# Kernel optimization log

Hardware: AMD Instinct MI355X
Metric: run time of the kernel (lower is better)

## Reference

```python
import jax, jax.numpy as jnp
import numpy as np

N_NODES = 50000
N_EDGES = 800000
H = 8            # n_heads
VAL_CH = 64      # h * n value channels
D = 3            # SO(3) degree dimension (2l+1, l=1)
T = 16           # key dim per head


def setup_inputs() -> dict:
    key = jax.random.key(0)
    k1, k2, k3, k4 = jax.random.split(key, 4)
    v = jax.random.normal(k1, (N_EDGES, VAL_CH, D), dtype=jnp.float32)
    k = jax.random.normal(k2, (N_EDGES, H, T), dtype=jnp.float32)
    q = jax.random.normal(k3, (N_NODES, H, T), dtype=jnp.float32)
    dst = jax.random.randint(k4, (N_EDGES,), 0, N_NODES, dtype=jnp.int32)
    return {"v": v, "k": k, "q": q, "dst": dst}


def reference(v, k, q, dst):
    # v: [E, h*n, d] edge values; k: [E, h, t] edge keys; q: [N, h, t] node queries
    E = v.shape[0]
    N = q.shape[0]
    h = k.shape[1]
    t = k.shape[2]
    vh = v.reshape(E, h, -1, v.shape[-1])          # [E, h, n, d]
    scale = 1.0 / np.sqrt(h * t).astype(np.float32)  # sqrt(f_key.deg_size)
    # per-edge attention logits: dot(k_e, q_dst(e)) per head
    logits = jnp.einsum('eht,eht->eh', k, q[dst]) * scale   # [E, h]
    # edge softmax over incoming edges of each destination node
    m = jax.ops.segment_max(logits, dst, num_segments=N)    # [N, h]
    m = jax.lax.stop_gradient(m)
    ex = jnp.exp(logits - m[dst])                           # [E, h]
    denom = jax.ops.segment_sum(ex, dst, num_segments=N)    # [N, h]
    a = ex / denom[dst]                                     # [E, h]
    # weighted message + scatter-sum to destination nodes
    msg = a[:, :, None, None] * vh                          # [E, h, n, d]
    out = jax.ops.segment_sum(msg, dst, num_segments=N)     # [N, h, n, d]
    return out.reshape(N, -1, v.shape[-1])                  # [N, h*n, d]
```

## Files before the change

kernel.cpp:

```cpp
#include <hip/hip_runtime.h>

#define HH 8
#define CAPL 128
#define BSTRIDE 256

static constexpr float SCALE = 0.08838834764831843f;

struct f3 {
  float x, y, z;
};

__device__ __forceinline__ float dot16(const float* kp, float4 q0, float4 q1,
                                       float4 q2, float4 q3) {
  const float4* k4 = (const float4*)kp;
  float4 a = k4[0], b = k4[1], c = k4[2], d = k4[3];
  float acc = a.x * q0.x + a.y * q0.y + a.z * q0.z + a.w * q0.w;
  acc += b.x * q1.x + b.y * q1.y + b.z * q1.z + b.w * q1.w;
  acc += c.x * q2.x + c.y * q2.y + c.z * q2.z + c.w * q2.w;
  acc += d.x * q3.x + d.y * q3.y + d.z * q3.z + d.w * q3.w;
  return acc;
}

__global__ __launch_bounds__(256) void fill_kernel(const int* __restrict__ dst,
                                                   int* __restrict__ cursor,
                                                   int* __restrict__ eid,
                                                   int E) {
  int e = blockIdx.x * blockDim.x + threadIdx.x;
  if (e >= E) return;
  int d = dst[e];
  int pos = atomicAdd(&cursor[d], 1);
  if (pos < BSTRIDE) eid[(size_t)d * BSTRIDE + pos] = e;
}

__global__ __launch_bounds__(256) void node_kernel(
    const float* __restrict__ v, const float* __restrict__ k,
    const float* __restrict__ q, const int* __restrict__ cursor,
    const int* __restrict__ eid, float* __restrict__ out, int N) {
  __shared__ int eidL[4][CAPL];
  __shared__ float wL[4][CAPL * HH];
  __shared__ float ovfL[4][HH];

  int tid = threadIdx.x;
  int wave = tid >> 6;
  int lane = tid & 63;
  int node = blockIdx.x * 4 + wave;
  if (node >= N) return;

  int deg = cursor[node];
  int nl = min(deg, CAPL);
  int nb = min(deg, BSTRIDE);
  const int* bucket = eid + (size_t)node * BSTRIDE;

  for (int i = lane; i < nl; i += 64) eidL[wave][i] = bucket[i];

  int h = lane & 7;
  int j = lane >> 3;

  const float4* qq = (const float4*)(q + (size_t)node * 128 + h * 16);
  float4 q0 = qq[0], q1 = qq[1], q2 = qq[2], q3 = qq[3];

  float m = -1e30f;
  for (int i = j; i < nl; i += 8) {
    int e = eidL[wave][i];
    float lg = dot16(k + (size_t)e * 128 + h * 16, q0, q1, q2, q3) * SCALE;
    wL[wave][i * 8 + h] = lg;
    m = fmaxf(m, lg);
  }
  for (int i = CAPL + j; i < nb; i += 8) {
    int e = bucket[i];
    float lg = dot16(k + (size_t)e * 128 + h * 16, q0, q1, q2, q3) * SCALE;
    m = fmaxf(m, lg);
  }
  m = fmaxf(m, __shfl_xor(m, 8, 64));
  m = fmaxf(m, __shfl_xor(m, 16, 64));
  m = fmaxf(m, __shfl_xor(m, 32, 64));

  float s = 0.f;
  for (int i = j; i < nl; i += 8) {
    float ex = __expf(wL[wave][i * 8 + h] - m);
    wL[wave][i * 8 + h] = ex;
    s += ex;
  }
  for (int i = CAPL + j; i < nb; i += 8) {
    int e = bucket[i];
    float lg = dot16(k + (size_t)e * 128 + h * 16, q0, q1, q2, q3) * SCALE;
    s += __expf(lg - m);
  }
  s += __shfl_xor(s, 8, 64);
  s += __shfl_xor(s, 16, 64);
  s += __shfl_xor(s, 32, 64);
  float inv = (s > 0.f) ? 1.0f / s : 0.f;

  int hc = lane >> 3;
  float minv = __shfl(inv, hc, 64);
  float a0 = 0.f, a1 = 0.f, a2 = 0.f;
  for (int i = 0; i < nl; ++i) {
    int e = eidL[wave][i];
    float w = wL[wave][i * 8 + hc];
    f3 vv = *(const f3*)(v + (size_t)e * 192 + lane * 3);
    a0 += w * vv.x;
    a1 += w * vv.y;
    a2 += w * vv.z;
  }
  for (int i = CAPL; i < nb; ++i) {
    int e = bucket[i];
    if (lane < 8) {
      float lg = dot16(k + (size_t)e * 128 + lane * 16, q0, q1, q2, q3) * SCALE;
      ovfL[wave][lane] = __expf(lg - m);
    }
    float w = ovfL[wave][hc];
    f3 vv = *(const f3*)(v + (size_t)e * 192 + lane * 3);
    a0 += w * vv.x;
    a1 += w * vv.y;
    a2 += w * vv.z;
  }
  a0 *= minv;
  a1 *= minv;
  a2 *= minv;

  f3* op = (f3*)(out + (size_t)node * 192 + lane * 3);
  op->x = a0;
  op->y = a1;
  op->z = a2;
}

extern "C" void kernel_launch(void* const* d_in, const int* in_sizes, int n_in,
                              void* d_out, int out_size, void* d_ws,
                              size_t ws_size, hipStream_t stream) {
  const float* v = (const float*)d_in[0];
  const float* k = (const float*)d_in[1];
  const float* q = (const float*)d_in[2];
  const int* dst = (const int*)d_in[3];
  float* out = (float*)d_out;

  const int E = in_sizes[3];
  const int N = in_sizes[2] / (HH * 16);

  char* ws = (char*)d_ws;
  int* cursor = (int*)ws;
  int* eid = (int*)(ws + (((size_t)N * 4 + 255) & ~(size_t)255));

  hipMemsetAsync(cursor, 0, (size_t)N * sizeof(int), stream);
  fill_kernel<<<(E + 255) / 256, 256, 0, stream>>>(dst, cursor, eid, E);
  node_kernel<<<(N + 3) / 4, 256, 0, stream>>>(v, k, q, cursor, eid, out, N);
}
```

Baseline: 310.5 us.

## Compute edge logits in bucket-fill kernel and store them per node slot

Per-edge attention logits are now computed in the bucketing kernel, with 8 threads per edge reading k contiguously via nontemporal loads, and written into a per-node slot array. The node kernel then reads those logits as coalesced data instead of gathering k rows by edge id and recomputing dot products, including for overflow edges. The value accumulation loop is also unrolled by four, using 32-bit offset arithmetic. The cost is an extra logit buffer written and read back (N*256*8 floats of workspace), and the overflow path is now simpler.

```diff
diff --git a/kernel.cpp b/kernel.cpp
--- a/kernel.cpp
+++ b/kernel.cpp
@@ -10,35 +10,48 @@
   float x, y, z;
 };
 
-__device__ __forceinline__ float dot16(const float* kp, float4 q0, float4 q1,
-                                       float4 q2, float4 q3) {
-  const float4* k4 = (const float4*)kp;
-  float4 a = k4[0], b = k4[1], c = k4[2], d = k4[3];
-  float acc = a.x * q0.x + a.y * q0.y + a.z * q0.z + a.w * q0.w;
-  acc += b.x * q1.x + b.y * q1.y + b.z * q1.z + b.w * q1.w;
-  acc += c.x * q2.x + c.y * q2.y + c.z * q2.z + c.w * q2.w;
-  acc += d.x * q3.x + d.y * q3.y + d.z * q3.z + d.w * q3.w;
-  return acc;
-}
+typedef float vf4 __attribute__((ext_vector_type(4)));
 
-__global__ __launch_bounds__(256) void fill_kernel(const int* __restrict__ dst,
-                                                   int* __restrict__ cursor,
-                                                   int* __restrict__ eid,
-                                                   int E) {
-  int e = blockIdx.x * blockDim.x + threadIdx.x;
+__global__ __launch_bounds__(256) void edge_kernel(
+    const float* __restrict__ k, const float* __restrict__ q,
+    const int* __restrict__ dst, int* __restrict__ cursor,
+    int* __restrict__ eid, float* __restrict__ lgS, int E) {
+  int t = blockIdx.x * 256 + threadIdx.x;
+  int e = t >> 3;
   if (e >= E) return;
+  int h = t & 7;
+  int lane = threadIdx.x & 63;
   int d = dst[e];
-  int pos = atomicAdd(&cursor[d], 1);
-  if (pos < BSTRIDE) eid[(size_t)d * BSTRIDE + pos] = e;
+
+  const vf4* kk = (const vf4*)(k + (size_t)e * 128 + h * 16);
+  const vf4* qq = (const vf4*)(q + (size_t)d * 128 + h * 16);
+  vf4 a0 = __builtin_nontemporal_load(kk + 0);
+  vf4 a1 = __builtin_nontemporal_load(kk + 1);
+  vf4 a2 = __builtin_nontemporal_load(kk + 2);
+  vf4 a3 = __builtin_nontemporal_load(kk + 3);
+  vf4 b0 = qq[0], b1 = qq[1], b2 = qq[2], b3 = qq[3];
+  float acc = a0.x * b0.x + a0.y * b0.y + a0.z * b0.z + a0.w * b0.w;
+  acc += a1.x * b1.x + a1.y * b1.y + a1.z * b1.z + a1.w * b1.w;
+  acc += a2.x * b2.x + a2.y * b2.y + a2.z * b2.z + a2.w * b2.w;
+  acc += a3.x * b3.x + a3.y * b3.y + a3.z * b3.z + a3.w * b3.w;
+  float lg = acc * SCALE;
+
+  int pos = 0;
+  if (h == 0) pos = atomicAdd(&cursor[d], 1);
+  pos = __shfl(pos, lane & ~7, 64);
+  if (pos < BSTRIDE) {
+    size_t slot = (size_t)d * BSTRIDE + pos;
+    if (h == 0) eid[slot] = e;
+    lgS[slot * HH + h] = lg;
+  }
 }
 
 __global__ __launch_bounds__(256) void node_kernel(
-    const float* __restrict__ v, const float* __restrict__ k,
-    const float* __restrict__ q, const int* __restrict__ cursor,
-    const int* __restrict__ eid, float* __restrict__ out, int N) {
+    const float* __restrict__ v, const float* __restrict__ lgS,
+    const int* __restrict__ cursor, const int* __restrict__ eid,
+    float* __restrict__ out, int N) {
   __shared__ int eidL[4][CAPL];
   __shared__ float wL[4][CAPL * HH];
-  __shared__ float ovfL[4][HH];
 
   int tid = threadIdx.x;
   int wave = tid >> 6;
@@ -46,46 +59,35 @@
   int node = blockIdx.x * 4 + wave;
   if (node >= N) return;
 
-  int deg = cursor[node];
+  int deg = min(cursor[node], BSTRIDE);
   int nl = min(deg, CAPL);
-  int nb = min(deg, BSTRIDE);
   const int* bucket = eid + (size_t)node * BSTRIDE;
+  const float* lgN = lgS + (size_t)node * (BSTRIDE * HH);
+  const char* vB = (const char*)v;
+  uint32_t vlane = (uint32_t)(lane * 12);
 
   for (int i = lane; i < nl; i += 64) eidL[wave][i] = bucket[i];
 
-  int h = lane & 7;
-  int j = lane >> 3;
-
-  const float4* qq = (const float4*)(q + (size_t)node * 128 + h * 16);
-  float4 q0 = qq[0], q1 = qq[1], q2 = qq[2], q3 = qq[3];
-
   float m = -1e30f;
-  for (int i = j; i < nl; i += 8) {
-    int e = eidL[wave][i];
-    float lg = dot16(k + (size_t)e * 128 + h * 16, q0, q1, q2, q3) * SCALE;
-    wL[wave][i * 8 + h] = lg;
+  for (int i = lane; i < nl * 8; i += 64) {
+    float lg = lgN[i];
+    wL[wave][i] = lg;
     m = fmaxf(m, lg);
   }
-  for (int i = CAPL + j; i < nb; i += 8) {
-    int e = bucket[i];
-    float lg = dot16(k + (size_t)e * 128 + h * 16, q0, q1, q2, q3) * SCALE;
-    m = fmaxf(m, lg);
-  }
+  for (int i = CAPL * 8 + lane; i < deg * 8; i += 64)
+    m = fmaxf(m, lgN[i]);
   m = fmaxf(m, __shfl_xor(m, 8, 64));
   m = fmaxf(m, __shfl_xor(m, 16, 64));
   m = fmaxf(m, __shfl_xor(m, 32, 64));
 
   float s = 0.f;
-  for (int i = j; i < nl; i += 8) {
-    float ex = __expf(wL[wave][i * 8 + h] - m);
-    wL[wave][i * 8 + h] = ex;
+  for (int i = lane; i < nl * 8; i += 64) {
+    float ex = __expf(wL[wave][i] - m);
+    wL[wave][i] = ex;
     s += ex;
   }
-  for (int i = CAPL + j; i < nb; i += 8) {
-    int e = bucket[i];
-    float lg = dot16(k + (size_t)e * 128 + h * 16, q0, q1, q2, q3) * SCALE;
-    s += __expf(lg - m);
-  }
+  for (int i = CAPL * 8 + lane; i < deg * 8; i += 64)
+    s += __expf(lgN[i] - m);
   s += __shfl_xor(s, 8, 64);
   s += __shfl_xor(s, 16, 64);
   s += __shfl_xor(s, 32, 64);
@@ -93,23 +95,38 @@
 
   int hc = lane >> 3;
   float minv = __shfl(inv, hc, 64);
+  float m_c = __shfl(m, hc, 64);
   float a0 = 0.f, a1 = 0.f, a2 = 0.f;
-  for (int i = 0; i < nl; ++i) {
+  int i = 0;
+  for (; i + 4 <= nl; i += 4) {
+    int e0 = eidL[wave][i + 0];
+    int e1 = eidL[wave][i + 1];
+    int e2 = eidL[wave][i + 2];
+    int e3 = eidL[wave][i + 3];
+    float w0 = wL[wave][(i + 0) * 8 + hc];
+    float w1 = wL[wave][(i + 1) * 8 + hc];
+    float w2 = wL[wave][(i + 2) * 8 + hc];
+    float w3 = wL[wave][(i + 3) * 8 + hc];
+    f3 v0 = *(const f3*)(vB + (uint32_t)e0 * 768u + vlane);
+    f3 v1 = *(const f3*)(vB + (uint32_t)e1 * 768u + vlane);
+    f3 v2 = *(const f3*)(vB + (uint32_t)e2 * 768u + vlane);
+    f3 v3 = *(const f3*)(vB + (uint32_t)e3 * 768u + vlane);
+    a0 += w0 * v0.x + w1 * v1.x + w2 * v2.x + w3 * v3.x;
+    a1 += w0 * v0.y + w1 * v1.y + w2 * v2.y + w3 * v3.y;
+    a2 += w0 * v0.z + w1 * v1.z + w2 * v2.z + w3 * v3.z;
+  }
+  for (; i < nl; ++i) {
     int e = eidL[wave][i];
     float w = wL[wave][i * 8 + hc];
-    f3 vv = *(const f3*)(v + (size_t)e * 192 + lane * 3);
+    f3 vv = *(const f3*)(vB + (uint32_t)e * 768u + vlane);
     a0 += w * vv.x;
     a1 += w * vv.y;
     a2 += w * vv.z;
   }
-  for (int i = CAPL; i < nb; ++i) {
+  for (; i < deg; ++i) {
     int e = bucket[i];
-    if (lane < 8) {
-      float lg = dot16(k + (size_t)e * 128 + lane * 16, q0, q1, q2, q3) * SCALE;
-      ovfL[wave][lane] = __expf(lg - m);
-    }
-    float w = ovfL[wave][hc];
-    f3 vv = *(const f3*)(v + (size_t)e * 192 + lane * 3);
+    float w = __expf(lgN[i * 8 + hc] - m_c);
+    f3 vv = *(const f3*)(vB + (uint32_t)e * 768u + vlane);
     a0 += w * vv.x;
     a1 += w * vv.y;
     a2 += w * vv.z;
@@ -118,7 +135,7 @@
   a1 *= minv;
   a2 *= minv;
 
-  f3* op = (f3*)(out + (size_t)node * 192 + lane * 3);
+  f3* op = (f3*)((char*)out + (uint32_t)node * 768u + vlane);
   op->x = a0;
   op->y = a1;
   op->z = a2;
@@ -137,10 +154,18 @@
   const int N = in_sizes[2] / (HH * 16);
 
   char* ws = (char*)d_ws;
-  int* cursor = (int*)ws;
-  int* eid = (int*)(ws + (((size_t)N * 4 + 255) & ~(size_t)255));
+  size_t off = 0;
+  auto take = [&](size_t bytes) {
+    void* p = ws + off;
+    off += (bytes + 255) & ~(size_t)255;
+    return p;
+  };
+  int* cursor = (int*)take((size_t)N * sizeof(int));
+  int* eid = (int*)take((size_t)N * BSTRIDE * sizeof(int));
+  float* lgS = (float*)take((size_t)N * BSTRIDE * HH * sizeof(float));
 
   hipMemsetAsync(cursor, 0, (size_t)N * sizeof(int), stream);
-  fill_kernel<<<(E + 255) / 256, 256, 0, stream>>>(dst, cursor, eid, E);
-  node_kernel<<<(N + 3) / 4, 256, 0, stream>>>(v, k, q, cursor, eid, out, N);
+  edge_kernel<<<(E * 8 + 255) / 256, 256, 0, stream>>>(k, q, dst, cursor, eid,
+                                                       lgS, E);
+  node_kernel<<<(N + 3) / 4, 256, 0, stream>>>(v, lgS, cursor, eid, out, N);
 }
```

Measured after the change: 318.9 us. +2.7%, slower.
